# Optimization experiments

Hardware: AMD Instinct MI355X
Metric: run time of the kernel (lower is better)

The kernel has to match this reference:

```python
import jax, jax.numpy as jnp
import numpy as np

EMBED = 768
HEADS = 8
HEAD_DIM = EMBED // HEADS  # 96


def setup_inputs() -> dict:
    key = jax.random.key(0)
    k1, k2, k3, k4, k5 = jax.random.split(key, 5)
    b, n = 4, 2048
    x = jax.random.normal(k1, (b, n, EMBED), dtype=jnp.float32)
    s = 1.0 / np.sqrt(EMBED)
    W_qkv = jax.random.normal(k2, (EMBED, 3 * EMBED), dtype=jnp.float32) * s
    b_qkv = jax.random.normal(k3, (3 * EMBED,), dtype=jnp.float32) * 0.02
    W_proj = jax.random.normal(k4, (EMBED, EMBED), dtype=jnp.float32) * s
    b_proj = jax.random.normal(k5, (EMBED,), dtype=jnp.float32) * 0.02
    return {"x": x, "W_qkv": W_qkv, "b_qkv": b_qkv, "W_proj": W_proj, "b_proj": b_proj}


def reference(x, W_qkv, b_qkv, W_proj, b_proj):
    b, n, _ = x.shape
    qkv = x @ W_qkv + b_qkv  # [b, n, 3*EMBED]
    # rearrange 'b n (h d qkv) -> qkv b h n d': qkv is fastest-varying axis
    qkv = qkv.reshape(b, n, HEADS, HEAD_DIM, 3)
    q = jnp.transpose(qkv[..., 0], (0, 2, 1, 3))  # [b, h, n, d]
    k = jnp.transpose(qkv[..., 1], (0, 2, 1, 3))
    v = jnp.transpose(qkv[..., 2], (0, 2, 1, 3))
    scale = 1.0 / np.sqrt(HEAD_DIM)
    energy = jnp.einsum('bhqd,bhkd->bhqk', q, k) * scale
    attn = jax.nn.softmax(energy, axis=-1)  # dropout p=0 -> identity
    out = jnp.einsum('bhqk,bhkd->bhqd', attn, v)
    out = jnp.transpose(out, (0, 2, 1, 3)).reshape(b, n, EMBED)
    out = out @ W_proj + b_proj
    return out
```

## Files before the change

### kernel.cpp

```cpp
#include <hip/hip_runtime.h>
#include <hip/hip_bf16.h>

#define EMBED 768
#define NHEADS 8
#define HDIM 96
#define SEQ 2048
#define BATCH 4
#define NTOK (BATCH*SEQ)
#define QKVN (3*EMBED)

#define QSCALE 0.14724444f

typedef __attribute__((ext_vector_type(4))) float f32x4;
typedef __attribute__((ext_vector_type(8))) __bf16 bf16x8;

__device__ __forceinline__ unsigned short f2bf(float f) {
  union { float f; unsigned int u; } c; c.f = f;
  unsigned int u = c.u;
  return (unsigned short)((u + 0x7FFFu + ((u >> 16) & 1u)) >> 16);
}

__device__ __forceinline__ unsigned int cvt_pk_bf16(float lo, float hi) {
  unsigned int r;
  asm("v_cvt_pk_bf16_f32 %0, %1, %2" : "=v"(r) : "v"(lo), "v"(hi));
  return r;
}

__device__ __forceinline__ void gload_lds16(const void* g, void* l) {
  __builtin_amdgcn_global_load_lds(
      (const __attribute__((address_space(1))) unsigned int*)g,
      (__attribute__((address_space(3))) unsigned int*)l, 16, 0, 0);
}

__global__ __launch_bounds__(256) void cast_x_kernel(const float4* __restrict__ in,
                                                     ushort4* __restrict__ out, int n4) {
  int i = blockIdx.x * 256 + threadIdx.x;
  if (i >= n4) return;
  float4 v = in[i];
  out[i] = make_ushort4(f2bf(v.x), f2bf(v.y), f2bf(v.z), f2bf(v.w));
}

__global__ __launch_bounds__(256) void transpose_cast_kernel(const float* __restrict__ in,
                                                             unsigned short* __restrict__ out,
                                                             int R, int C, int remap) {
  __shared__ float t[32][33];
  int c0 = blockIdx.x * 32, r0 = blockIdx.y * 32;
  int tx = threadIdx.x & 31, ty = threadIdx.x >> 5;
  #pragma unroll
  for (int i = 0; i < 32; i += 8)
    t[ty + i][tx] = in[(size_t)(r0 + ty + i) * C + c0 + tx];
  __syncthreads();
  #pragma unroll
  for (int i = 0; i < 32; i += 8) {
    int c = c0 + ty + i;
    int rp = remap ? (c % 3) * 768 + c / 3 : c;
    out[(size_t)rp * R + r0 + tx] = f2bf(t[tx][ty + i]);
  }
}

template <int MODE>
__global__ __launch_bounds__(256) void gemm_kernel(
    const unsigned short* __restrict__ A, const unsigned short* __restrict__ B,
    const float* __restrict__ bias, int K,
    unsigned short* __restrict__ Qo, unsigned short* __restrict__ Ko,
    unsigned short* __restrict__ Vt, float* __restrict__ out) {
  __shared__ unsigned short As[2][128][32];
  __shared__ unsigned short Bs[2][128][32];
  const int tid = threadIdx.x;
  const int lane = tid & 63, wid = tid >> 6;
  const int wr = wid >> 1, wc = wid & 1;
  const int l15 = lane & 15, l16 = lane >> 4;
  const int m0 = blockIdx.y * 128, n0 = blockIdx.x * 128;

  auto stage = [&](int buf, int k0) {
    #pragma unroll
    for (int i = 0; i < 2; i++) {
      int chunk = i * 256 + tid;
      gload_lds16(A + (size_t)(m0 + (chunk >> 2)) * K + k0 + (chunk & 3) * 8,
                  (char*)&As[buf][0][0] + (i * 256 + wid * 64) * 16);
      gload_lds16(B + (size_t)(n0 + (chunk >> 2)) * K + k0 + (chunk & 3) * 8,
                  (char*)&Bs[buf][0][0] + (i * 256 + wid * 64) * 16);
    }
  };

  f32x4 acc[4][4] = {};

  stage(0, 0);
  __syncthreads();
  int cur = 0;
  for (int k0 = 0; k0 < K; k0 += 32, cur ^= 1) {
    if (k0 + 32 < K) stage(cur ^ 1, k0 + 32);

    bf16x8 af[4], bfr[4];
    #pragma unroll
    for (int mi = 0; mi < 4; mi++)
      af[mi] = *(const bf16x8*)&As[cur][wr * 64 + mi * 16 + l15][l16 * 8];
    #pragma unroll
    for (int ni = 0; ni < 4; ni++)
      bfr[ni] = *(const bf16x8*)&Bs[cur][wc * 64 + ni * 16 + l15][l16 * 8];
    #pragma unroll
    for (int mi = 0; mi < 4; mi++)
      #pragma unroll
      for (int ni = 0; ni < 4; ni++)
        acc[mi][ni] = __builtin_amdgcn_mfma_f32_16x16x32_bf16(af[mi], bfr[ni], acc[mi][ni], 0, 0, 0);

    __syncthreads();
  }

  if (MODE == 0) {
    #pragma unroll
    for (int mi = 0; mi < 4; mi++) {
      #pragma unroll
      for (int ni = 0; ni < 4; ni++) {
        int base = n0 + wc * 64 + ni * 16;
        int which = base / 768;
        int hd = base - which * 768;
        int h = hd / 96;
        int d0 = hd - h * 96;
        float bb = bias[hd * 3 + which + 3 * l15];
        #pragma unroll
        for (int j = 0; j < 4; j++) {
          int row = m0 + wr * 64 + mi * 16 + l16 * 4 + j;
          int bi = row >> 11, nn = row & 2047;
          float v = acc[mi][ni][j] + bb;
          size_t bh = (size_t)(bi * NHEADS + h);
          if (which == 0)      Qo[(bh * SEQ + nn) * HDIM + d0 + l15] = f2bf(v * QSCALE);
          else if (which == 1) Ko[(bh * SEQ + nn) * HDIM + d0 + l15] = f2bf(v);
          else {
            int nn2 = (nn & ~63) | (nn & 32) | ((nn & 12) << 1) | ((nn & 16) >> 2) | (nn & 3);
            Vt[(bh * HDIM + d0 + l15) * SEQ + nn2] = f2bf(v);
          }
        }
      }
    }
  } else {
    #pragma unroll
    for (int mi = 0; mi < 4; mi++) {
      #pragma unroll
      for (int ni = 0; ni < 4; ni++) {
        int col = n0 + wc * 64 + ni * 16 + l15;
        float bb = bias[col];
        #pragma unroll
        for (int j = 0; j < 4; j++) {
          int row = m0 + wr * 64 + mi * 16 + l16 * 4 + j;
          out[(size_t)row * EMBED + col] = acc[mi][ni][j] + bb;
        }
      }
    }
  }
}

__global__ __launch_bounds__(256) void attn_kernel(
    const unsigned short* __restrict__ Q, const unsigned short* __restrict__ Kd,
    const unsigned short* __restrict__ Vt, unsigned short* __restrict__ Oa) {
  __shared__ unsigned short Ks[2][64 * 96];
  __shared__ unsigned short Vs[2][96 * 64];

  const int tid = threadIdx.x, lane = tid & 63, wid = tid >> 6;
  const int l15 = lane & 15, l16 = lane >> 4;
  const int bid = blockIdx.x;
  const int swz = (bid & 7) * 64 + (bid >> 3);
  const int qb_ = swz & 15, bh = swz >> 4;
  const int bi = bh >> 3, h = bh & 7;
  const int q0 = qb_ * 128;

  const unsigned short* Qg = Q + ((size_t)bh * SEQ + q0) * HDIM;
  const unsigned short* Kg = Kd + (size_t)bh * SEQ * HDIM;
  const unsigned short* Vg = Vt + (size_t)bh * HDIM * SEQ;

  bf16x8 qf[2][3];
  #pragma unroll
  for (int qb = 0; qb < 2; qb++)
    #pragma unroll
    for (int ks = 0; ks < 3; ks++)
      qf[qb][ks] = *(const bf16x8*)(Qg + (size_t)(wid * 32 + qb * 16 + l15) * HDIM + ks * 32 + l16 * 8);

  auto stageKV = [&](int buf, int k0) {
    #pragma unroll
    for (int i = 0; i < 3; i++) {
      int idx = i * 256 + tid;
      gload_lds16(Kg + (size_t)k0 * HDIM + idx * 8,
                  (char*)&Ks[buf][0] + (i * 256 + wid * 64) * 16);
    }
    #pragma unroll
    for (int i = 0; i < 3; i++) {
      int idx = i * 256 + tid;
      int d = idx >> 3, s = idx & 7;
      gload_lds16(Vg + (size_t)d * SEQ + k0 + ((s ^ (d & 7)) << 3),
                  (char*)&Vs[buf][0] + (i * 256 + wid * 64) * 16);
    }
  };

  f32x4 oacc[2][6] = {};
  float mrow[2], lrow[2];
  mrow[0] = mrow[1] = -__builtin_inff();
  lrow[0] = lrow[1] = 0.f;

  stageKV(0, 0);
  __syncthreads();

  for (int kb = 0; kb < SEQ / 64; kb++) {
    const int cur = kb & 1;
    if (kb + 1 < SEQ / 64) stageKV(cur ^ 1, (kb + 1) * 64);

    const char* Kc = (const char*)&Ks[cur][0];
    const char* Vc = (const char*)&Vs[cur][0];

    f32x4 sacc[2][4] = {};
    #pragma unroll
    for (int ks = 0; ks < 3; ks++) {
      bf16x8 ak[4];
      #pragma unroll
      for (int ni = 0; ni < 4; ni++)
        ak[ni] = *(const bf16x8*)(Kc + (ni * 16 + l15) * 192 + ks * 64 + l16 * 16);
      #pragma unroll
      for (int qb = 0; qb < 2; qb++)
        #pragma unroll
        for (int ni = 0; ni < 4; ni++)
          sacc[qb][ni] = __builtin_amdgcn_mfma_f32_16x16x32_bf16(ak[ni], qf[qb][ks], sacc[qb][ni], 0, 0, 0);
    }

    float tmax[2];
    float g = -3.4e38f;
    #pragma unroll
    for (int qb = 0; qb < 2; qb++) {
      float a0 = fmaxf(fmaxf(sacc[qb][0][0], sacc[qb][0][1]), fmaxf(sacc[qb][0][2], sacc[qb][0][3]));
      float a1 = fmaxf(fmaxf(sacc[qb][1][0], sacc[qb][1][1]), fmaxf(sacc[qb][1][2], sacc[qb][1][3]));
      float a2 = fmaxf(fmaxf(sacc[qb][2][0], sacc[qb][2][1]), fmaxf(sacc[qb][2][2], sacc[qb][2][3]));
      float a3 = fmaxf(fmaxf(sacc[qb][3][0], sacc[qb][3][1]), fmaxf(sacc[qb][3][2], sacc[qb][3][3]));
      float v = fmaxf(fmaxf(a0, a1), fmaxf(a2, a3));
      v = fmaxf(v, __shfl_xor(v, 16));
      v = fmaxf(v, __shfl_xor(v, 32));
      tmax[qb] = v;
      g = fmaxf(g, v - mrow[qb]);
    }
    if (!__all(g <= 11.54f)) {
      #pragma unroll
      for (int qb = 0; qb < 2; qb++) {
        float mnew = fmaxf(mrow[qb], tmax[qb]);
        float alpha = __builtin_amdgcn_exp2f(mrow[qb] - mnew);
        mrow[qb] = mnew;
        lrow[qb] *= alpha;
        #pragma unroll
        for (int d6 = 0; d6 < 6; d6++) {
          oacc[qb][d6][0] *= alpha; oacc[qb][d6][1] *= alpha;
          oacc[qb][d6][2] *= alpha; oacc[qb][d6][3] *= alpha;
        }
      }
    }

    unsigned int pk[2][8];
    #pragma unroll
    for (int qb = 0; qb < 2; qb++) {
      const float m = mrow[qb];
      float psum = 0.f;
      #pragma unroll
      for (int ni = 0; ni < 4; ni++) {
        float p0 = __builtin_amdgcn_exp2f(sacc[qb][ni][0] - m);
        float p1 = __builtin_amdgcn_exp2f(sacc[qb][ni][1] - m);
        float p2 = __builtin_amdgcn_exp2f(sacc[qb][ni][2] - m);
        float p3 = __builtin_amdgcn_exp2f(sacc[qb][ni][3] - m);
        psum += (p0 + p1) + (p2 + p3);
        pk[qb][ni * 2]     = cvt_pk_bf16(p0, p1);
        pk[qb][ni * 2 + 1] = cvt_pk_bf16(p2, p3);
      }
      psum += __shfl_xor(psum, 16);
      psum += __shfl_xor(psum, 32);
      lrow[qb] += psum;
    }

    #pragma unroll
    for (int ks = 0; ks < 2; ks++) {
      bf16x8 vb[6];
      #pragma unroll
      for (int d6 = 0; d6 < 6; d6++)
        vb[d6] = *(const bf16x8*)(Vc + (d6 * 16 + l15) * 128 +
                                  (((ks * 4 + l16) ^ (l15 & 7)) << 4));
      #pragma unroll
      for (int qb = 0; qb < 2; qb++) {
        union { unsigned int u[4]; bf16x8 v; } pf;
        pf.u[0] = pk[qb][4 * ks];     pf.u[1] = pk[qb][4 * ks + 1];
        pf.u[2] = pk[qb][4 * ks + 2]; pf.u[3] = pk[qb][4 * ks + 3];
        #pragma unroll
        for (int d6 = 0; d6 < 6; d6++)
          oacc[qb][d6] = __builtin_amdgcn_mfma_f32_16x16x32_bf16(vb[d6], pf.v, oacc[qb][d6], 0, 0, 0);
      }
    }

    __syncthreads();
  }

  #pragma unroll
  for (int qb = 0; qb < 2; qb++) {
    const float rl = 1.f / lrow[qb];
    const int tok = q0 + wid * 32 + qb * 16 + l15;
    unsigned short* Og = Oa + ((size_t)bi * SEQ + tok) * EMBED + h * HDIM;
    #pragma unroll
    for (int d6 = 0; d6 < 6; d6++) {
      uint2 o;
      o.x = cvt_pk_bf16(oacc[qb][d6][0] * rl, oacc[qb][d6][1] * rl);
      o.y = cvt_pk_bf16(oacc[qb][d6][2] * rl, oacc[qb][d6][3] * rl);
      *(uint2*)(Og + d6 * 16 + l16 * 4) = o;
    }
  }
}

extern "C" void kernel_launch(void* const* d_in, const int* in_sizes, int n_in,
                              void* d_out, int out_size, void* d_ws, size_t ws_size,
                              hipStream_t stream) {
  const float* x      = (const float*)d_in[0];
  const float* W_qkv  = (const float*)d_in[1];
  const float* b_qkv  = (const float*)d_in[2];
  const float* W_proj = (const float*)d_in[3];
  const float* b_proj = (const float*)d_in[4];
  float* out = (float*)d_out;

  char* ws = (char*)d_ws;
  size_t off = 0;
  auto alloc = [&](size_t bytes) { void* p = ws + off; off += (bytes + 255) & ~(size_t)255; return p; };
  unsigned short* xb  = (unsigned short*)alloc((size_t)NTOK * EMBED * 2);
  unsigned short* WqT = (unsigned short*)alloc((size_t)QKVN * EMBED * 2);
  unsigned short* WpT = (unsigned short*)alloc((size_t)EMBED * EMBED * 2);
  unsigned short* Qb  = (unsigned short*)alloc((size_t)NTOK * EMBED * 2);
  unsigned short* Kb  = (unsigned short*)alloc((size_t)NTOK * EMBED * 2);
  unsigned short* Vtb = (unsigned short*)alloc((size_t)NTOK * EMBED * 2);
  unsigned short* Ob  = (unsigned short*)alloc((size_t)NTOK * EMBED * 2);

  cast_x_kernel<<<dim3(NTOK * EMBED / 4 / 256), dim3(256), 0, stream>>>(
      (const float4*)x, (ushort4*)xb, NTOK * EMBED / 4);
  transpose_cast_kernel<<<dim3(QKVN / 32, EMBED / 32), dim3(256), 0, stream>>>(W_qkv, WqT, EMBED, QKVN, 1);
  transpose_cast_kernel<<<dim3(EMBED / 32, EMBED / 32), dim3(256), 0, stream>>>(W_proj, WpT, EMBED, EMBED, 0);

  gemm_kernel<0><<<dim3(QKVN / 128, NTOK / 128), dim3(256), 0, stream>>>(
      xb, WqT, b_qkv, EMBED, Qb, Kb, Vtb, nullptr);

  attn_kernel<<<dim3(BATCH * NHEADS * (SEQ / 128)), dim3(256), 0, stream>>>(Qb, Kb, Vtb, Ob);

  gemm_kernel<1><<<dim3(EMBED / 128, NTOK / 128), dim3(256), 0, stream>>>(
      Ob, WpT, b_proj, EMBED, nullptr, nullptr, nullptr, out);
}
```

Before: 184.5 us.

## Restructure GEMM with 64-wide K tiles, XOR-swizzled LDS, XCD block remap

```diff
diff --git a/kernel.cpp b/kernel.cpp
--- a/kernel.cpp
+++ b/kernel.cpp
@@ -59,52 +59,75 @@
 }
 
 template <int MODE>
-__global__ __launch_bounds__(256) void gemm_kernel(
+__global__ __launch_bounds__(256, 2) void gemm8_kernel(
     const unsigned short* __restrict__ A, const unsigned short* __restrict__ B,
-    const float* __restrict__ bias, int K,
+    const float* __restrict__ bias, int K, int NB,
     unsigned short* __restrict__ Qo, unsigned short* __restrict__ Ko,
     unsigned short* __restrict__ Vt, float* __restrict__ out) {
-  __shared__ unsigned short As[2][128][32];
-  __shared__ unsigned short Bs[2][128][32];
+  __shared__ unsigned short As[2][128 * 64];
+  __shared__ unsigned short Bs[2][128 * 64];
   const int tid = threadIdx.x;
   const int lane = tid & 63, wid = tid >> 6;
   const int wr = wid >> 1, wc = wid & 1;
   const int l15 = lane & 15, l16 = lane >> 4;
-  const int m0 = blockIdx.y * 128, n0 = blockIdx.x * 128;
-
-  auto stage = [&](int buf, int k0) {
-    #pragma unroll
-    for (int i = 0; i < 2; i++) {
-      int chunk = i * 256 + tid;
-      gload_lds16(A + (size_t)(m0 + (chunk >> 2)) * K + k0 + (chunk & 3) * 8,
-                  (char*)&As[buf][0][0] + (i * 256 + wid * 64) * 16);
-      gload_lds16(B + (size_t)(n0 + (chunk >> 2)) * K + k0 + (chunk & 3) * 8,
-                  (char*)&Bs[buf][0][0] + (i * 256 + wid * 64) * 16);
+  const int cpx = gridDim.x >> 3;
+  const int bid = blockIdx.x;
+  const int swz = (bid & 7) * cpx + (bid >> 3);
+  const int my = swz / NB, nx = swz - my * NB;
+  const int m0 = my * 128, n0 = nx * 128;
+
+  auto stage_half = [&](int buf, int kt, int half) {
+    const unsigned short* src = half ? B : A;
+    const int base0 = half ? n0 : m0;
+    char* dst = (char*)(half ? &Bs[buf][0] : &As[buf][0]);
+    #pragma unroll
+    for (int i = 0; i < 4; i++) {
+      int c = i * 256 + tid;
+      int r = c >> 3, s = c & 7;
+      gload_lds16(src + (size_t)(base0 + r) * K + kt * 64 + ((s ^ (r & 7)) << 3),
+                  dst + (i * 256 + wid * 64) * 16);
     }
   };
 
   f32x4 acc[4][4] = {};
-
-  stage(0, 0);
-  __syncthreads();
-  int cur = 0;
-  for (int k0 = 0; k0 < K; k0 += 32, cur ^= 1) {
-    if (k0 + 32 < K) stage(cur ^ 1, k0 + 32);
-
-    bf16x8 af[4], bfr[4];
-    #pragma unroll
-    for (int mi = 0; mi < 4; mi++)
-      af[mi] = *(const bf16x8*)&As[cur][wr * 64 + mi * 16 + l15][l16 * 8];
-    #pragma unroll
-    for (int ni = 0; ni < 4; ni++)
-      bfr[ni] = *(const bf16x8*)&Bs[cur][wc * 64 + ni * 16 + l15][l16 * 8];
-    #pragma unroll
-    for (int mi = 0; mi < 4; mi++)
+  const int xr = (l15 & 7) << 4;
+
+  stage_half(0, 0, 0);
+  stage_half(0, 0, 1);
+  asm volatile("s_waitcnt vmcnt(0)" ::: "memory");
+  __builtin_amdgcn_s_barrier();
+
+  const int NT = K >> 6;
+  for (int t = 0; t < NT; ++t) {
+    const int cur = t & 1;
+    const char* Ac = (const char*)&As[cur][0];
+    const char* Bc = (const char*)&Bs[cur][0];
+    #pragma unroll
+    for (int kh = 0; kh < 2; ++kh) {
+      bf16x8 af[4], bfr[4];
+      #pragma unroll
+      for (int mi = 0; mi < 4; mi++)
+        af[mi] = *(const bf16x8*)(Ac + (wr * 64 + mi * 16 + l15) * 128 +
+                                  ((kh * 64 + l16 * 16) ^ xr));
       #pragma unroll
       for (int ni = 0; ni < 4; ni++)
-        acc[mi][ni] = __builtin_amdgcn_mfma_f32_16x16x32_bf16(af[mi], bfr[ni], acc[mi][ni], 0, 0, 0);
-
-    __syncthreads();
+        bfr[ni] = *(const bf16x8*)(Bc + (wc * 64 + ni * 16 + l15) * 128 +
+                                   ((kh * 64 + l16 * 16) ^ xr));
+      if (t + 1 < NT) stage_half(cur ^ 1, t + 1, kh);
+      __builtin_amdgcn_s_barrier();
+      __builtin_amdgcn_s_setprio(1);
+      #pragma unroll
+      for (int mi = 0; mi < 4; mi++)
+        #pragma unroll
+        for (int ni = 0; ni < 4; ni++)
+          acc[mi][ni] = __builtin_amdgcn_mfma_f32_16x16x32_bf16(af[mi], bfr[ni], acc[mi][ni], 0, 0, 0);
+      __builtin_amdgcn_s_setprio(0);
+      __builtin_amdgcn_s_barrier();
+    }
+    asm volatile("s_waitcnt lgkmcnt(0)" ::: "memory");
+    asm volatile("s_waitcnt vmcnt(0)" ::: "memory");
+    __builtin_amdgcn_sched_barrier(0);
+    __builtin_amdgcn_s_barrier();
   }
 
   if (MODE == 0) {
@@ -117,18 +140,25 @@
         int hd = base - which * 768;
         int h = hd / 96;
         int d0 = hd - h * 96;
-        float bb = bias[hd * 3 + which + 3 * l15];
-        #pragma unroll
-        for (int j = 0; j < 4; j++) {
-          int row = m0 + wr * 64 + mi * 16 + l16 * 4 + j;
-          int bi = row >> 11, nn = row & 2047;
-          float v = acc[mi][ni][j] + bb;
-          size_t bh = (size_t)(bi * NHEADS + h);
-          if (which == 0)      Qo[(bh * SEQ + nn) * HDIM + d0 + l15] = f2bf(v * QSCALE);
-          else if (which == 1) Ko[(bh * SEQ + nn) * HDIM + d0 + l15] = f2bf(v);
-          else {
-            int nn2 = (nn & ~63) | (nn & 32) | ((nn & 12) << 1) | ((nn & 16) >> 2) | (nn & 3);
-            Vt[(bh * HDIM + d0 + l15) * SEQ + nn2] = f2bf(v);
+        float bb = bias[(hd + l15) * 3 + which];
+        int rowb = m0 + wr * 64 + mi * 16 + l16 * 4;
+        int bi = rowb >> 11, nnb = rowb & 2047;
+        size_t bh = (size_t)(bi * NHEADS + h);
+        if (which == 2) {
+          int nn2 = (nnb & ~63) | (nnb & 32) | ((nnb & 12) << 1) | ((nnb & 16) >> 2) | (nnb & 3);
+          float v0 = acc[mi][ni][0] + bb, v1 = acc[mi][ni][1] + bb;
+          float v2 = acc[mi][ni][2] + bb, v3 = acc[mi][ni][3] + bb;
+          uint2 pk;
+          pk.x = cvt_pk_bf16(v0, v1);
+          pk.y = cvt_pk_bf16(v2, v3);
+          *(uint2*)(Vt + (bh * HDIM + d0 + l15) * SEQ + nn2) = pk;
+        } else {
+          #pragma unroll
+          for (int j = 0; j < 4; j++) {
+            float v = acc[mi][ni][j] + bb;
+            int nn = nnb + j;
+            if (which == 0) Qo[(bh * SEQ + nn) * HDIM + d0 + l15] = f2bf(v * QSCALE);
+            else            Ko[(bh * SEQ + nn) * HDIM + d0 + l15] = f2bf(v);
           }
         }
       }
@@ -331,11 +361,11 @@
   transpose_cast_kernel<<<dim3(QKVN / 32, EMBED / 32), dim3(256), 0, stream>>>(W_qkv, WqT, EMBED, QKVN, 1);
   transpose_cast_kernel<<<dim3(EMBED / 32, EMBED / 32), dim3(256), 0, stream>>>(W_proj, WpT, EMBED, EMBED, 0);
 
-  gemm_kernel<0><<<dim3(QKVN / 128, NTOK / 128), dim3(256), 0, stream>>>(
-      xb, WqT, b_qkv, EMBED, Qb, Kb, Vtb, nullptr);
+  gemm8_kernel<0><<<dim3((NTOK / 128) * (QKVN / 128)), dim3(256), 0, stream>>>(
+      xb, WqT, b_qkv, EMBED, QKVN / 128, Qb, Kb, Vtb, nullptr);
 
   attn_kernel<<<dim3(BATCH * NHEADS * (SEQ / 128)), dim3(256), 0, stream>>>(Qb, Kb, Vtb, Ob);
 
-  gemm_kernel<1><<<dim3(EMBED / 128, NTOK / 128), dim3(256), 0, stream>>>(
-      Ob, WpT, b_proj, EMBED, nullptr, nullptr, nullptr, out);
-}
+  gemm8_kernel<1><<<dim3((NTOK / 128) * (EMBED / 128)), dim3(256), 0, stream>>>(
+      Ob, WpT, b_proj, EMBED, EMBED / 128, nullptr, nullptr, nullptr, out);
+}
```

After: 157.6 us. 1.17x faster.
